# Performance work log

Hardware: AMD Instinct MI355X
Metric: run time of the kernel (lower is better)

Reference implementation:

```python
import jax, jax.numpy as jnp
import numpy as np
from jax import lax

H = 1024
W = 1024
WIN = 32
STR = 16
NH = (H - WIN) // STR + 1  # 63
N = NH * NH                # 3969 patches
DN3 = ('NCDHW', 'OIDHW', 'NCDHW')
DN2 = ('NCHW', 'OIHW', 'NCHW')


def setup_inputs() -> dict:
    key = jax.random.key(0)
    ks = jax.random.split(key, 13)
    r = lambda k, s, sc=0.05: jax.random.normal(k, s, dtype=jnp.float32) * sc
    return {
        'x1': jax.random.normal(ks[0], (1, 1, 1, H, W), jnp.float32),
        'x2': jax.random.normal(ks[1], (1, 1, 1, H, W), jnp.float32),
        'conv1_w': r(ks[2], (24, 1, 2, 8, 8)),      # Conv3d(1,24,(2,8,8)) [O,I,D,H,W]
        'conv1_b': r(ks[3], (24,)),
        'conv2_w': r(ks[4], (60, 24, 5, 5)),         # Conv2d(24,60,5)
        'conv2_b': r(ks[5], (60,)),
        'deconv2_w': r(ks[6], (60, 24, 5, 5)),       # ConvTranspose2d(60,24,5) [I,O,kH,kW]
        'deconv2_b': r(ks[7], (24,)),
        'deconv1_w': r(ks[8], (24, 1, 2, 8, 8)),     # ConvTranspose3d(24,1,(2,8,8)) [I,O,D,H,W]
        'deconv1_b': r(ks[9], (1,)),
        'lin_w': r(ks[10], (N, 2), 0.5),             # per-patch Linear(2,1) weights
        'lin_b': r(ks[11], (N,), 0.5),               # per-patch Linear(2,1) bias
        'linear1_w': r(ks[12], (1, 1), 0.5),         # Linear(1,1,bias=False)
    }


def _conv(x, w, b, dn):
    nd = w.ndim - 2
    y = lax.conv_general_dilated(x, w, (1,) * nd, 'VALID', dimension_numbers=dn)
    return y + b.reshape((1, -1) + (1,) * nd)


def _convT(x, w, b, dn):
    # stride-1, pad-0 transposed conv == full-pad conv with flipped, IO-swapped kernel
    nd = w.ndim - 2
    wf = jnp.flip(w, axis=tuple(range(2, w.ndim))).swapaxes(0, 1)  # [O,I,*k]
    pad = [(k - 1, k - 1) for k in w.shape[2:]]
    y = lax.conv_general_dilated(x, wf, (1,) * nd, pad, dimension_numbers=dn)
    return y + b.reshape((1, -1) + (1,) * nd)


def reference(x1, x2, conv1_w, conv1_b, conv2_w, conv2_b, deconv2_w, deconv2_b,
              deconv1_w, deconv1_b, lin_w, lin_b, linear1_w):
    x = jnp.concatenate([x1, x2], axis=2)[0, 0]  # [2,H,W]
    idx = (jnp.arange(NH) * STR)[:, None] + jnp.arange(WIN)[None, :]  # [NH,32]
    # unfold dims 3,4 with window 32 / stride 16 -> [2,NH,NW,32,32]
    patches = x[:, idx[:, None, :, None], idx[None, :, None, :]]
    outX = patches.reshape(2, N, WIN, WIN).transpose(1, 0, 2, 3)[:, None]  # [N,1,2,32,32]
    h = jax.nn.elu(_conv(outX, conv1_w, conv1_b, DN3))        # [N,24,1,25,25]
    h = jax.nn.relu(_conv(h[:, :, 0], conv2_w, conv2_b, DN2))  # [N,60,21,21]
    h = jax.nn.elu(_convT(h, deconv2_w, deconv2_b, DN2))       # [N,24,25,25]
    h = _convT(h[:, :, None], deconv1_w, deconv1_b, DN3)       # [N,1,2,32,32]
    # per-patch Linear(2,1) over depth channels, batched over all patches
    p = jnp.einsum('nchw,nc->nhw', h[:, 0], lin_w) + lin_b[:, None, None]  # [N,32,32]
    p = p.reshape(NH, NH, WIN, WIN)
    # col2im: overlap-add fold, block 32, stride 16 -> [H,W]
    recon = jnp.zeros((H, W), jnp.float32).at[idx[:, None, :, None], idx[None, :, None, :]].add(p)
    outX2 = recon * linear1_w[0, 0]  # Linear(1,1,bias=False) per pixel
    return x2 - outX2.reshape(x2.shape)
```

## Files before the change

kernel.cpp:

```cpp
#include <hip/hip_runtime.h>
#include <hip/hip_bf16.h>

static constexpr int H_ = 1024;
static constexpr int W_ = 1024;
static constexpr int STR_ = 16;
static constexpr int NH_ = 63;
static constexpr int NPATCH_ = NH_ * NH_;

typedef short bf16x8 __attribute__((ext_vector_type(8)));
typedef short short4v __attribute__((ext_vector_type(4)));
typedef float f32x4 __attribute__((ext_vector_type(4)));

static constexpr int SH1_STRIDE = 48;
static constexpr int SH2_BASE   = 30016;
static constexpr int SH2_STRIDE = 120;
static constexpr int ZROW_REL   = 441 * SH2_STRIDE;
static constexpr int SPB0       = 30016;
static constexpr int SPB1       = 35136;
static constexpr int SWC_BASE   = 30016;
static constexpr int SP_ACC     = 34112;
static constexpr int LDS_BYTES  = 83072;

__device__ __forceinline__ unsigned short f2bf(float x) {
    __hip_bfloat16 b = __float2bfloat16(x);
    return __builtin_bit_cast(unsigned short, b);
}

__device__ __forceinline__ f32x4 mfma_bf16(bf16x8 a, bf16x8 b, f32x4 c) {
    return __builtin_amdgcn_mfma_f32_16x16x32_bf16(a, b, c, 0, 0, 0);
}

__device__ __forceinline__ float elu_neg(float x) { return __expf(x) - 1.f; }

__global__ __launch_bounds__(1024, 4) void fused_patch_kernel(
    const float* __restrict__ x1, const float* __restrict__ x2,
    const float* __restrict__ c1b, const float* __restrict__ c2b,
    const float* __restrict__ d2b, const float* __restrict__ d1b,
    const float* __restrict__ lin_w, const float* __restrict__ lin_b,
    const unsigned short* __restrict__ w1frag,
    const unsigned short* __restrict__ w2frag,
    const unsigned short* __restrict__ dw2frag,
    const float* __restrict__ dw1,
    float* __restrict__ recon)
{
    __shared__ alignas(16) char sbuf[LDS_BYTES];
    const int n  = blockIdx.x;
    const int t  = (int)threadIdx.x;
    const int pi = n / NH_, pj = n % NH_;
    const int Y0 = pi * STR_, X0 = pj * STR_;
    const int wv = t >> 6, lane = t & 63;
    const int ln15 = lane & 15, quad = lane >> 4;

    bf16x8 w1b[8];
    #pragma unroll
    for (int g = 0; g < 8; ++g)
        w1b[g] = *(const bf16x8*)(w1frag + (g * 64 + lane) * 8);
    const float lw0  = lin_w[2 * n], lw1 = lin_w[2 * n + 1];
    const float lbn  = lin_b[n];
    const float d1b0 = d1b[0];
    const float c1b0 = c1b[ln15];
    const float c1b1 = (16 + ln15 < 24) ? c1b[16 + ln15] : 0.f;
    float c2bias[4];
    #pragma unroll
    for (int nt = 0; nt < 4; ++nt) {
        int o = nt * 16 + ln15;
        c2bias[nt] = (o < 60) ? c2b[o] : 0.f;
    }
    const float db0 = d2b[ln15];
    const float db1 = (16 + ln15 < 24) ? d2b[16 + ln15] : 0.f;
    float dwp[4] = {0.f, 0.f, 0.f, 0.f};
    {
        int r0 = t >> 5, c0 = t & 31;
        if (c0 < 24) {
            dwp[0] = dw1[(c0 * 2 + 0) * 64 + r0];
            dwp[1] = dw1[(c0 * 2 + 1) * 64 + r0];
        }
        int k1 = t + 1024, r1 = k1 >> 5, c1 = k1 & 31;
        if (c1 < 24) {
            dwp[2] = dw1[(c1 * 2 + 0) * 64 + r1];
            dwp[3] = dw1[(c1 * 2 + 1) * 64 + r1];
        }
    }

    if (t < 30)      ((float*)(sbuf + SH2_BASE + ZROW_REL))[t] = 0.f;
    else if (t < 34) ((float*)(sbuf + 30000))[t - 30] = 0.f;
    else if (t < 38) ((float*)(sbuf + SH2_BASE + 53040))[t - 34] = 0.f;
    for (int k = t; k < 2048; k += 1024) {
        int d = k >> 10, r = k & 1023, y = r >> 5, x = r & 31;
        unsigned short b = f2bf((d ? x2 : x1)[(Y0 + y) * W_ + (X0 + x)]);
        int row = (d * 32 + y) * 40;
        ((unsigned short*)(sbuf + SPB0))[row + x] = b;
        if (x > 0) ((unsigned short*)(sbuf + SPB1))[row + x - 1] = b;
    }
    __syncthreads();

    for (int tl = wv; tl < 50; tl += 16) {
        const int vcol = tl >> 1, ubase = (tl & 1) * 16;
        const int u = ubase + ln15;
        const char* abase = sbuf + ((vcol & 1) ? SPB1 : SPB0) + (vcol & ~1) * 2;
        f32x4 acc[2];
        acc[0] = (f32x4){0.f, 0.f, 0.f, 0.f};
        acc[1] = (f32x4){0.f, 0.f, 0.f, 0.f};
        #pragma unroll
        for (int kc = 0; kc < 4; ++kc) {
            const int idx8 = kc * 4 + quad;
            const int dd = idx8 >> 3, pp = idx8 & 7;
            const unsigned int* ap = (const unsigned int*)(abase + (dd * 32 + u + pp) * 80);
            union { unsigned int u4[4]; bf16x8 v; } af;
            af.u4[0] = ap[0]; af.u4[1] = ap[1]; af.u4[2] = ap[2]; af.u4[3] = ap[3];
            acc[0] = mfma_bf16(af.v, w1b[kc * 2 + 0], acc[0]);
            acc[1] = mfma_bf16(af.v, w1b[kc * 2 + 1], acc[1]);
        }
        #pragma unroll
        for (int ntp = 0; ntp < 2; ++ntp) {
            const int c = ntp * 16 + ln15;
            if (c < 24) {
                const float bias = ntp ? c1b1 : c1b0;
                #pragma unroll
                for (int r = 0; r < 4; ++r) {
                    int uu = ubase + quad * 4 + r;
                    if (uu < 25) {
                        float hv = acc[ntp][r] + bias;
                        hv = hv > 0.f ? hv : elu_neg(hv);
                        *(unsigned short*)(sbuf + (uu * 25 + vcol) * SH1_STRIDE + c * 2) = f2bf(hv);
                    }
                }
            }
        }
    }
    __syncthreads();

    if (wv < 14) {
        int abase2[2];
        #pragma unroll
        for (int i = 0; i < 2; ++i) {
            int m = (wv + i * 14) * 16 + ln15;
            if (m > 440) m = 440;
            abase2[i] = ((m / 21) * 25 + (m % 21)) * SH1_STRIDE;
        }
        f32x4 acc2[2][4];
        #pragma unroll
        for (int i = 0; i < 2; ++i)
            #pragma unroll
            for (int nt = 0; nt < 4; ++nt)
                acc2[i][nt] = (f32x4){0.f, 0.f, 0.f, 0.f};

        const unsigned short* wb = w2frag + lane * 8;
        bf16x8 A0[2], A1[2], BA[4], BB[4];

#define S2_LDA(TAP, DST) do { \
        const int to_ = ((((TAP) / 5) * 25) + ((TAP) % 5)) * SH1_STRIDE; \
        _Pragma("unroll") \
        for (int i_ = 0; i_ < 2; ++i_) \
            DST[i_] = *(const bf16x8*)(sbuf + abase2[i_] + to_ + quad * 16); \
    } while (0)
#define S2_LDB(TAP, DST) do { \
        _Pragma("unroll") \
        for (int nt_ = 0; nt_ < 4; ++nt_) \
            DST[nt_] = *(const bf16x8*)(wb + ((TAP) * 4 + nt_) * 512); \
    } while (0)
#define S2_MM(AR, BR) do { \
        _Pragma("unroll") \
        for (int i_ = 0; i_ < 2; ++i_) { \
            _Pragma("unroll") \
            for (int nt_ = 0; nt_ < 4; ++nt_) \
                acc2[i_][nt_] = mfma_bf16(AR[i_], BR[nt_], acc2[i_][nt_]); \
        } \
    } while (0)

        S2_LDB(0, BA); S2_LDB(1, BB);
        S2_LDA(0, A0); S2_LDA(1, A1);
        #pragma unroll 1
        for (int tp = 0; tp < 24; tp += 2) {
            S2_MM(A0, BA);
            S2_LDA(tp + 2, A0);
            S2_LDB(tp + 2, BA);
            S2_MM(A1, BB);
            const int t3 = (tp + 3 > 24) ? 24 : (tp + 3);
            S2_LDA(t3, A1);
            S2_LDB(t3, BB);
        }
        S2_MM(A0, BA);

        #pragma unroll
        for (int i = 0; i < 2; ++i) {
            #pragma unroll
            for (int r = 0; r < 4; ++r) {
                int pix = (wv + i * 14) * 16 + quad * 4 + r;
                if (pix < 441) {
                    unsigned short* rowp = (unsigned short*)(sbuf + SH2_BASE + pix * SH2_STRIDE);
                    #pragma unroll
                    for (int nt = 0; nt < 4; ++nt) {
                        int o = nt * 16 + ln15;
                        if (o < 60)
                            rowp[o] = f2bf(fmaxf(acc2[i][nt][r] + c2bias[nt], 0.f));
                    }
                }
            }
        }
    }
    __syncthreads();

    f32x4 acc3[3][2];
    {
        #pragma unroll
        for (int i = 0; i < 3; ++i) {
            acc3[i][0] = (f32x4){0.f, 0.f, 0.f, 0.f};
            acc3[i][1] = (f32x4){0.f, 0.f, 0.f, 0.f};
        }
        int uarr[3], varr[3], a120[3];
        bool mval[3];
        #pragma unroll
        for (int i = 0; i < 3; ++i) {
            int m = (wv + i * 16) * 16 + ln15;
            mval[i] = (m < 625);
            int mc = mval[i] ? m : 0;
            uarr[i] = mc / 25; varr[i] = mc % 25;
            a120[i] = (uarr[i] * 21 + varr[i]) * SH2_STRIDE;
        }
        const unsigned short* db = dw2frag + lane * 8;

#define S3_LDB(TAP, DST) do { \
        _Pragma("unroll") \
        for (int f_ = 0; f_ < 4; ++f_) \
            DST[f_] = *(const bf16x8*)(db + ((TAP) * 4 + f_) * 512); \
    } while (0)
#define S3_TAP(TAP, BR, NI_) do { \
        const int dy_ = (TAP) / 5, dx_ = (TAP) % 5; \
        const int t2o_ = (dy_ * 21 + dx_) * SH2_STRIDE; \
        bf16x8 a0_[NI_], a1_[NI_]; \
        _Pragma("unroll") \
        for (int i_ = 0; i_ < NI_; ++i_) { \
            int yv_ = uarr[i_] - dy_, xv_ = varr[i_] - dx_; \
            bool ok_ = mval[i_] && ((unsigned)yv_ < 21u) && ((unsigned)xv_ < 21u); \
            int ra_ = ok_ ? (a120[i_] - t2o_) : ZROW_REL;   \
            const char* ap_ = sbuf + SH2_BASE + ra_ + quad * 16; \
            short4v lo0_ = *(const short4v*)(ap_); \
            short4v hi0_ = *(const short4v*)(ap_ + 8); \
            a0_[i_] = __builtin_shufflevector(lo0_, hi0_, 0, 1, 2, 3, 4, 5, 6, 7); \
            short4v lo1_ = *(const short4v*)(ap_ + 64); \
            short4v hi1_ = *(const short4v*)(ap_ + 72); \
            a1_[i_] = __builtin_shufflevector(lo1_, hi1_, 0, 1, 2, 3, 4, 5, 6, 7); \
        } \
        _Pragma("unroll") \
        for (int i_ = 0; i_ < NI_; ++i_) { \
            acc3[i_][0] = mfma_bf16(a0_[i_], BR[0], acc3[i_][0]); \
            acc3[i_][1] = mfma_bf16(a0_[i_], BR[1], acc3[i_][1]); \
            acc3[i_][0] = mfma_bf16(a1_[i_], BR[2], acc3[i_][0]); \
            acc3[i_][1] = mfma_bf16(a1_[i_], BR[3], acc3[i_][1]); \
        } \
    } while (0)
#define S3_SWEEP(NI_) do { \
        bf16x8 BA[4], BB[4]; \
        S3_LDB(0, BA); S3_LDB(1, BB); \
        _Pragma("unroll 1") \
        for (int tp = 0; tp < 24; tp += 2) { \
            S3_TAP(tp, BA, NI_); \
            S3_LDB(tp + 2, BA); \
            S3_TAP(tp + 1, BB, NI_); \
            const int t3_ = (tp + 3 > 24) ? 24 : (tp + 3); \
            S3_LDB(t3_, BB); \
        } \
        S3_TAP(24, BA, NI_); \
    } while (0)

        if (wv < 8) { S3_SWEEP(3); } else { S3_SWEEP(2); }
    }
    __syncthreads();

    float* sp = (float*)(sbuf + SP_ACC);
    {
        const int c1ok = (16 + ln15 < 24);
        #pragma unroll
        for (int i = 0; i < 3; ++i) {
            if (i == 2 && wv >= 8) continue;
            #pragma unroll
            for (int r = 0; r < 4; ++r) {
                int pix = (wv + i * 16) * 16 + quad * 4 + r;
                if (pix < 625) {
                    unsigned short* rowp = (unsigned short*)(sbuf + pix * SH1_STRIDE);
                    float hv = acc3[i][0][r] + db0;
                    rowp[ln15] = f2bf(hv > 0.f ? hv : elu_neg(hv));
                    if (c1ok) {
                        float hw = acc3[i][1][r] + db1;
                        rowp[16 + ln15] = f2bf(hw > 0.f ? hw : elu_neg(hw));
                    }
                }
            }
        }
    }
    {
        int r0 = t >> 5, c0 = t & 31;
        ((unsigned short*)(sbuf + SWC_BASE))[r0 * 32 + c0] = f2bf(lw0 * dwp[0] + lw1 * dwp[1]);
        int k1 = t + 1024, r1 = k1 >> 5, c1 = k1 & 31;
        ((unsigned short*)(sbuf + SWC_BASE))[r1 * 32 + c1] = f2bf(lw0 * dwp[2] + lw1 * dwp[3]);
    }
    sp[t] = 0.f;
    __syncthreads();

    {
        bf16x8 wbv[4];
        int ntoff[4];
        #pragma unroll
        for (int nt = 0; nt < 4; ++nt) {
            wbv[nt] = *(const bf16x8*)(sbuf + SWC_BASE + (nt * 16 + ln15) * 64 + quad * 16);
            int rv = nt * 16 + ln15;
            ntoff[nt] = (rv >> 3) * 32 + (rv & 7);
        }
        #pragma unroll
        for (int i = 0; i < 3; ++i) {
            int mt = wv + i * 16;
            if (mt >= 40) continue;
            int m = mt * 16 + ln15;
            if (m > 624) m = 624;
            bf16x8 a = *(const bf16x8*)(sbuf + m * SH1_STRIDE + quad * 16);
            int uvb[4];
            bool pok[4];
            #pragma unroll
            for (int r = 0; r < 4; ++r) {
                int pix = mt * 16 + quad * 4 + r;
                pok[r] = (pix < 625);
                int pc = pok[r] ? pix : 0;
                uvb[r] = (pc / 25) * 32 + (pc % 25);
            }
            #pragma unroll
            for (int nt = 0; nt < 4; ++nt) {
                f32x4 acc4 = (f32x4){0.f, 0.f, 0.f, 0.f};
                acc4 = mfma_bf16(a, wbv[nt], acc4);
                #pragma unroll
                for (int r = 0; r < 4; ++r) {
                    if (pok[r])
                        atomicAdd(&sp[uvb[r] + ntoff[nt]], acc4[r]);
                }
            }
        }
    }
    __syncthreads();

    const float obias = d1b0 * (lw0 + lw1) + lbn;
    {
        int yy = t >> 5, xx = t & 31;
        atomicAdd(&recon[(Y0 + yy) * W_ + (X0 + xx)], sp[t] + obias);
    }
}

__global__ void prep_kernel(const float* __restrict__ c1w,
                            const float* __restrict__ c2w,
                            const float* __restrict__ d2w,
                            unsigned short* __restrict__ w1frag,
                            unsigned short* __restrict__ w2frag,
                            unsigned short* __restrict__ dw2frag)
{
    int i = blockIdx.x * blockDim.x + threadIdx.x;
    if (i < 51200) {
        int j = i & 7, lane = (i >> 3) & 63;
        int ln15 = lane & 15, quad = lane >> 4;
        if (i < 4096) {
            int g = i >> 9;
            int kc = g >> 1, nt = g & 1;
            int nn = nt * 16 + ln15, k = kc * 32 + quad * 8 + j;
            w1frag[i] = f2bf((nn < 24) ? c1w[nn * 128 + k] : 0.f);
        }
        {
            int nt = (i >> 9) & 3, tap = i >> 11;
            int o = nt * 16 + ln15, c = quad * 8 + j;
            float v = (o < 60 && c < 24) ? c2w[(o * 24 + c) * 25 + tap] : 0.f;
            w2frag[i] = f2bf(v);
        }
        {
            int nt = (i >> 9) & 1, kc = (i >> 10) & 1, tap = i >> 11;
            int k = kc * 32 + quad * 8 + j, c = nt * 16 + ln15;
            float v = (k < 60 && c < 24) ? d2w[(k * 24 + c) * 25 + tap] : 0.f;
            dw2frag[i] = f2bf(v);
        }
    }
}

__global__ void finalize_kernel(const float* __restrict__ x2,
                                const float* __restrict__ l1w,
                                float* __restrict__ out)
{
    int i = blockIdx.x * blockDim.x + threadIdx.x;
    if (i < H_ * W_) {
        float r = out[i];
        out[i] = x2[i] - r * l1w[0];
    }
}

extern "C" void kernel_launch(void* const* d_in, const int* in_sizes, int n_in,
                              void* d_out, int out_size, void* d_ws, size_t ws_size,
                              hipStream_t stream)
{
    const float* x1  = (const float*)d_in[0];
    const float* x2  = (const float*)d_in[1];
    const float* c1w = (const float*)d_in[2];
    const float* c1b = (const float*)d_in[3];
    const float* c2w = (const float*)d_in[4];
    const float* c2b = (const float*)d_in[5];
    const float* d2w = (const float*)d_in[6];
    const float* d2b = (const float*)d_in[7];
    const float* d1w = (const float*)d_in[8];
    const float* d1b = (const float*)d_in[9];
    const float* lw  = (const float*)d_in[10];
    const float* lb  = (const float*)d_in[11];
    const float* l1w = (const float*)d_in[12];

    float*          out     = (float*)d_out;
    unsigned short* w1frag  = (unsigned short*)d_ws;
    unsigned short* w2frag  = (unsigned short*)((char*)d_ws + 8192);
    unsigned short* dw2frag = (unsigned short*)((char*)d_ws + 110592);

    hipMemsetAsync(d_out, 0, (size_t)H_ * W_ * sizeof(float), stream);
    prep_kernel<<<100, 512, 0, stream>>>(c1w, c2w, d2w, w1frag, w2frag, dw2frag);
    fused_patch_kernel<<<NPATCH_, 1024, 0, stream>>>(x1, x2, c1b, c2b, d2b, d1b,
                                                     lw, lb, w1frag, w2frag, dw2frag,
                                                     d1w, out);
    finalize_kernel<<<(H_ * W_ + 255) / 256, 256, 0, stream>>>(x2, l1w, out);
}
```

Before: 1.390 ms.

## Stage conv2 and deconv2 weight fragments through LDS in tap chunks

Replaces per-wave global loads of the conv2 and deconv2 B-fragments with cooperative block-wide copies into a new LDS staging region, done in three chunks of taps with barriers around each. Each wave then reads its weights from LDS instead of global/L2. This grows LDS use from about 83 KB to 120 KB per block and adds several __syncthreads. It also drops the previous software double-buffering of weight loads, so the stages may lose latency overlap and occupancy.

```diff
diff --git a/kernel.cpp b/kernel.cpp
--- a/kernel.cpp
+++ b/kernel.cpp
@@ -19,7 +19,8 @@
 static constexpr int SPB1       = 35136;
 static constexpr int SWC_BASE   = 30016;
 static constexpr int SP_ACC     = 34112;
-static constexpr int LDS_BYTES  = 83072;
+static constexpr int SW_STAGE   = 83072;
+static constexpr int LDS_BYTES  = 119936;
 
 __device__ __forceinline__ unsigned short f2bf(float x) {
     __hip_bfloat16 b = __float2bfloat16(x);
@@ -82,6 +83,13 @@
         }
     }
 
+    auto stageB = [&](const unsigned short* srcw, int tapBase, int nTaps) {
+        const f32x4* src = (const f32x4*)(srcw + tapBase * 2048);
+        f32x4* dst = (f32x4*)(sbuf + SW_STAGE);
+        const int nv = nTaps * 256;
+        for (int i = t; i < nv; i += 1024) dst[i] = src[i];
+    };
+
     if (t < 30)      ((float*)(sbuf + SH2_BASE + ZROW_REL))[t] = 0.f;
     else if (t < 34) ((float*)(sbuf + 30000))[t - 30] = 0.f;
     else if (t < 38) ((float*)(sbuf + SH2_BASE + 53040))[t - 34] = 0.f;
@@ -130,58 +138,48 @@
     }
     __syncthreads();
 
+    int abase2[2];
+    #pragma unroll
+    for (int i = 0; i < 2; ++i) {
+        int m = (wv + i * 14) * 16 + ln15;
+        if (m > 440) m = 440;
+        abase2[i] = ((m / 21) * 25 + (m % 21)) * SH1_STRIDE;
+    }
+    f32x4 acc2[2][4];
+    #pragma unroll
+    for (int i = 0; i < 2; ++i)
+        #pragma unroll
+        for (int nt = 0; nt < 4; ++nt)
+            acc2[i][nt] = (f32x4){0.f, 0.f, 0.f, 0.f};
+
+    auto computeS2 = [&](int tapBase, int nTaps) {
+        if (wv >= 14) return;
+        const char* sW = sbuf + SW_STAGE;
+        for (int tl = 0; tl < nTaps; ++tl) {
+            const int tap  = tapBase + tl;
+            const int toff = ((tap / 5) * 25 + (tap % 5)) * SH1_STRIDE;
+            bf16x8 b[4];
+            #pragma unroll
+            for (int nt = 0; nt < 4; ++nt)
+                b[nt] = *(const bf16x8*)(sW + (tl * 4 + nt) * 1024 + lane * 16);
+            #pragma unroll
+            for (int i = 0; i < 2; ++i) {
+                bf16x8 a = *(const bf16x8*)(sbuf + abase2[i] + toff + quad * 16);
+                #pragma unroll
+                for (int nt = 0; nt < 4; ++nt)
+                    acc2[i][nt] = mfma_bf16(a, b[nt], acc2[i][nt]);
+            }
+        }
+    };
+
+    stageB(w2frag, 0, 9);   __syncthreads();
+    computeS2(0, 9);        __syncthreads();
+    stageB(w2frag, 9, 8);   __syncthreads();
+    computeS2(9, 8);        __syncthreads();
+    stageB(w2frag, 17, 8);  __syncthreads();
+    computeS2(17, 8);
+
     if (wv < 14) {
-        int abase2[2];
-        #pragma unroll
-        for (int i = 0; i < 2; ++i) {
-            int m = (wv + i * 14) * 16 + ln15;
-            if (m > 440) m = 440;
-            abase2[i] = ((m / 21) * 25 + (m % 21)) * SH1_STRIDE;
-        }
-        f32x4 acc2[2][4];
-        #pragma unroll
-        for (int i = 0; i < 2; ++i)
-            #pragma unroll
-            for (int nt = 0; nt < 4; ++nt)
-                acc2[i][nt] = (f32x4){0.f, 0.f, 0.f, 0.f};
-
-        const unsigned short* wb = w2frag + lane * 8;
-        bf16x8 A0[2], A1[2], BA[4], BB[4];
-
-#define S2_LDA(TAP, DST) do { \
-        const int to_ = ((((TAP) / 5) * 25) + ((TAP) % 5)) * SH1_STRIDE; \
-        _Pragma("unroll") \
-        for (int i_ = 0; i_ < 2; ++i_) \
-            DST[i_] = *(const bf16x8*)(sbuf + abase2[i_] + to_ + quad * 16); \
-    } while (0)
-#define S2_LDB(TAP, DST) do { \
-        _Pragma("unroll") \
-        for (int nt_ = 0; nt_ < 4; ++nt_) \
-            DST[nt_] = *(const bf16x8*)(wb + ((TAP) * 4 + nt_) * 512); \
-    } while (0)
-#define S2_MM(AR, BR) do { \
-        _Pragma("unroll") \
-        for (int i_ = 0; i_ < 2; ++i_) { \
-            _Pragma("unroll") \
-            for (int nt_ = 0; nt_ < 4; ++nt_) \
-                acc2[i_][nt_] = mfma_bf16(AR[i_], BR[nt_], acc2[i_][nt_]); \
-        } \
-    } while (0)
-
-        S2_LDB(0, BA); S2_LDB(1, BB);
-        S2_LDA(0, A0); S2_LDA(1, A1);
-        #pragma unroll 1
-        for (int tp = 0; tp < 24; tp += 2) {
-            S2_MM(A0, BA);
-            S2_LDA(tp + 2, A0);
-            S2_LDB(tp + 2, BA);
-            S2_MM(A1, BB);
-            const int t3 = (tp + 3 > 24) ? 24 : (tp + 3);
-            S2_LDA(t3, A1);
-            S2_LDB(t3, BB);
-        }
-        S2_MM(A0, BA);
-
         #pragma unroll
         for (int i = 0; i < 2; ++i) {
             #pragma unroll
@@ -218,16 +216,16 @@
             uarr[i] = mc / 25; varr[i] = mc % 25;
             a120[i] = (uarr[i] * 21 + varr[i]) * SH2_STRIDE;
         }
-        const unsigned short* db = dw2frag + lane * 8;
-
-#define S3_LDB(TAP, DST) do { \
+        const char* sW = sbuf + SW_STAGE;
+
+#define S3_TAP(TAPBASE, TL, NI_) do { \
+        const int tap_ = (TAPBASE) + (TL); \
+        const int dy_ = tap_ / 5, dx_ = tap_ % 5; \
+        const int t2o_ = (dy_ * 21 + dx_) * SH2_STRIDE; \
+        bf16x8 bc_[4]; \
         _Pragma("unroll") \
         for (int f_ = 0; f_ < 4; ++f_) \
-            DST[f_] = *(const bf16x8*)(db + ((TAP) * 4 + f_) * 512); \
-    } while (0)
-#define S3_TAP(TAP, BR, NI_) do { \
-        const int dy_ = (TAP) / 5, dx_ = (TAP) % 5; \
-        const int t2o_ = (dy_ * 21 + dx_) * SH2_STRIDE; \
+            bc_[f_] = *(const bf16x8*)(sW + ((TL) * 4 + f_) * 1024 + lane * 16); \
         bf16x8 a0_[NI_], a1_[NI_]; \
         _Pragma("unroll") \
         for (int i_ = 0; i_ < NI_; ++i_) { \
@@ -244,27 +242,26 @@
         } \
         _Pragma("unroll") \
         for (int i_ = 0; i_ < NI_; ++i_) { \
-            acc3[i_][0] = mfma_bf16(a0_[i_], BR[0], acc3[i_][0]); \
-            acc3[i_][1] = mfma_bf16(a0_[i_], BR[1], acc3[i_][1]); \
-            acc3[i_][0] = mfma_bf16(a1_[i_], BR[2], acc3[i_][0]); \
-            acc3[i_][1] = mfma_bf16(a1_[i_], BR[3], acc3[i_][1]); \
+            acc3[i_][0] = mfma_bf16(a0_[i_], bc_[0], acc3[i_][0]); \
+            acc3[i_][1] = mfma_bf16(a0_[i_], bc_[1], acc3[i_][1]); \
+            acc3[i_][0] = mfma_bf16(a1_[i_], bc_[2], acc3[i_][0]); \
+            acc3[i_][1] = mfma_bf16(a1_[i_], bc_[3], acc3[i_][1]); \
         } \
     } while (0)
-#define S3_SWEEP(NI_) do { \
-        bf16x8 BA[4], BB[4]; \
-        S3_LDB(0, BA); S3_LDB(1, BB); \
-        _Pragma("unroll 1") \
-        for (int tp = 0; tp < 24; tp += 2) { \
-            S3_TAP(tp, BA, NI_); \
-            S3_LDB(tp + 2, BA); \
-            S3_TAP(tp + 1, BB, NI_); \
-            const int t3_ = (tp + 3 > 24) ? 24 : (tp + 3); \
-            S3_LDB(t3_, BB); \
+#define S3_CHUNK(TAPBASE, NTAPS) do { \
+        if (wv < 8) { \
+            for (int tl_ = 0; tl_ < (NTAPS); ++tl_) S3_TAP(TAPBASE, tl_, 3); \
+        } else { \
+            for (int tl_ = 0; tl_ < (NTAPS); ++tl_) S3_TAP(TAPBASE, tl_, 2); \
         } \
-        S3_TAP(24, BA, NI_); \
     } while (0)
 
-        if (wv < 8) { S3_SWEEP(3); } else { S3_SWEEP(2); }
+        stageB(dw2frag, 0, 9);   __syncthreads();
+        S3_CHUNK(0, 9);          __syncthreads();
+        stageB(dw2frag, 9, 8);   __syncthreads();
+        S3_CHUNK(9, 8);          __syncthreads();
+        stageB(dw2frag, 17, 8);  __syncthreads();
+        S3_CHUNK(17, 8);
     }
     __syncthreads();
 
```

New measurement: 1.406 ms. No clear change (+1.1%).
